# Kernel optimization log

Hardware: AMD Instinct MI355X
Metric: run time of the kernel (lower is better)

## Reference

```python
import jax, jax.numpy as jnp
import numpy as np

FRONT, END = 1, 2            # COMBINE_FRONT / COMBINE_END label values
BOS_ID, EOS_ID = 0, 1
BS, SLEN, D, H, L = 16, 256, 1024, 16, 2
N_POS = 512                  # N_MAX_POSITIONS


def setup_inputs():
    key = jax.random.key(0)
    ks = iter(jax.random.split(key, 80))
    nrm = lambda shape: jax.random.normal(next(ks), shape, dtype=jnp.float32) * 0.02
    inp = {}
    inp["encoded"] = jax.random.normal(next(ks), (BS, SLEN, D), dtype=jnp.float32)
    inp["lengths"] = jnp.full((BS,), SLEN, dtype=jnp.int32)  # assert slen == lengths.max()
    # deterministic valid word-span labels: [F,F,F,E,O,F,E,O] repeated -> words of 4 and 2 subwords
    pat = np.tile(np.array([1, 1, 1, 2, 0, 1, 2, 0], dtype=np.int32), SLEN // 8)
    inp["combine_labels"] = jnp.asarray(np.broadcast_to(pat, (BS, SLEN)).copy())
    inp["lang_id"] = 0
    inp["pos_emb"] = nrm((N_POS, D))
    inp["special_emb"] = nrm((3, D)).at[2].set(0.0)  # padding_idx=2 row zeroed
    for p in ("ctx", "wc"):
        for w in ("Wq", "Wk", "Wv", "Wo"):
            inp[p + "_" + w] = nrm((L, D, D))
        for b in ("bq", "bk", "bv", "bo", "b2", "be1", "be2"):
            inp[p + "_" + b] = jnp.zeros((L, D), dtype=jnp.float32)
        inp[p + "_W1"] = nrm((L, D, 4 * D))
        inp[p + "_b1"] = jnp.zeros((L, 4 * D), dtype=jnp.float32)
        inp[p + "_W2"] = nrm((L, 4 * D, D))
        inp[p + "_g1"] = jnp.ones((L, D), dtype=jnp.float32)
        inp[p + "_g2"] = jnp.ones((L, D), dtype=jnp.float32)
    return inp


def _ln(x, g, b):
    m = x.mean(-1, keepdims=True)
    v = ((x - m) ** 2).mean(-1, keepdims=True)
    return (x - m) / jnp.sqrt(v + 1e-5) * g + b


def _encoder(x, pad, P):
    # post-norm TransformerEncoder (torch default): attn -> add&LN -> relu-FFN -> add&LN
    Wq, Wk, Wv, Wo, bq, bk, bv, bo, W1, b1, W2, b2, g1, be1, g2, be2 = P
    B, S, Dm = x.shape
    hd = Dm // H
    scale = 1.0 / np.sqrt(hd)
    for i in range(Wq.shape[0]):
        q = (x @ Wq[i] + bq[i]).reshape(B, S, H, hd)
        k = (x @ Wk[i] + bk[i]).reshape(B, S, H, hd)
        v = (x @ Wv[i] + bv[i]).reshape(B, S, H, hd)
        s = jnp.einsum("bqhd,bkhd->bhqk", q, k) * scale
        s = jnp.where(pad[:, None, None, :], -1e9, s)  # src_key_padding_mask
        a = jax.nn.softmax(s, axis=-1)
        o = jnp.einsum("bhqk,bkhd->bqhd", a, v).reshape(B, S, Dm) @ Wo[i] + bo[i]
        x = _ln(x + o, g1[i], be1[i])
        h = jax.nn.relu(x @ W1[i] + b1[i]) @ W2[i] + b2[i]
        x = _ln(x + h, g2[i], be2[i])
    return x


def _word_inputs(encoded, combine_labels, special_emb):
    # vectorized replacement of the nested python-loop ragged span builder;
    # index math on the (concrete) labels in numpy, gathers/scatters in jnp.
    cl = np.asarray(combine_labels)
    f = cl == FRONT
    e = cl == END
    c = np.cumsum(f.astype(np.int64), axis=1)
    frontrun = c - np.maximum.accumulate(np.where(f, 0, c), axis=1)  # run of FRONTs ending here
    fr_prev = np.pad(frontrun[:, :-1], ((0, 0), (1, 0)))
    slot = np.where(f, frontrun, fr_prev + 1)  # 1-based slot inside word (slot 0 = BOS)
    e_flat = e.reshape(-1)
    wid = np.cumsum(e_flat) - e_flat  # word id = #ENDs strictly before, row-major order
    tok_idx = np.nonzero((f | e).reshape(-1))[0]
    w_tok = wid[tok_idx]
    s_tok = slot.reshape(-1)[tok_idx]
    wlen = fr_prev[e] + 3  # k subwords (fr_prev+1) + BOS + EOS
    n_word = wlen.shape[0]
    maxL = int(wlen.max())
    Dm = encoded.shape[-1]
    x = jnp.zeros((n_word, maxL, Dm), dtype=encoded.dtype)
    x = x.at[:, 0].set(special_emb[BOS_ID])
    x = x.at[np.arange(n_word), wlen - 1].set(special_emb[EOS_ID])  # eos at slot k+1
    x = x.at[w_tok, s_tok].set(encoded.reshape(-1, Dm)[tok_idx])
    return x, wlen


def _forward(encoded, lengths, combine_labels, pos_emb, special_emb, ctx, wc):
    S = encoded.shape[1]
    pad = jnp.asarray(np.arange(S)[None, :] >= np.asarray(lengths)[:, None])
    x = _encoder(encoded + pos_emb[:S][None], pad, ctx)          # another_encode
    winp, wlen = _word_inputs(x, combine_labels, special_emb)    # ragged gather, [n_word, maxL, D]
    maxL = winp.shape[1]
    wpad = jnp.asarray(np.arange(maxL)[None, :] >= wlen[:, None])
    y = _encoder(winp + pos_emb[:maxL][None], wpad, wc)          # word_encode
    return y[:, 0]  # position-0 (BOS) representation, [n_word, D]


def reference(encoded, lengths, combine_labels, lang_id, pos_emb, special_emb,
              ctx_Wq, ctx_Wk, ctx_Wv, ctx_Wo, ctx_bq, ctx_bk, ctx_bv, ctx_bo,
              ctx_W1, ctx_b1, ctx_W2, ctx_b2, ctx_g1, ctx_be1, ctx_g2, ctx_be2,
              wc_Wq, wc_Wk, wc_Wv, wc_Wo, wc_bq, wc_bk, wc_bv, wc_bo,
              wc_W1, wc_b1, wc_W2, wc_b2, wc_g1, wc_be1, wc_g2, wc_be2):
    ctx = (ctx_Wq, ctx_Wk, ctx_Wv, ctx_Wo, ctx_bq, ctx_bk, ctx_bv, ctx_bo,
           ctx_W1, ctx_b1, ctx_W2, ctx_b2, ctx_g1, ctx_be1, ctx_g2, ctx_be2)
    wc = (wc_Wq, wc_Wk, wc_Wv, wc_Wo, wc_bq, wc_bk, wc_bv, wc_bo,
          wc_W1, wc_b1, wc_W2, wc_b2, wc_g1, wc_be1, wc_g2, wc_be2)
    return _forward(encoded, lengths, combine_labels, pos_emb, special_emb, ctx, wc)
```

## Files before the change

kernel.cpp:

```cpp
#include <hip/hip_runtime.h>
#include <stdint.h>

typedef unsigned short u16;
typedef __attribute__((ext_vector_type(8))) short short8;
typedef __attribute__((ext_vector_type(4))) short short4v;
typedef __attribute__((ext_vector_type(4))) float f32x4;

#define DEV static __device__ __forceinline__

constexpr int B = 16, S = 256, D = 1024, H = 16, LYR = 2, FF = 4096;
constexpr int Mc = B * S;
constexpr int MAXL = 6;
constexpr int QKVS = 3 * D;

DEV u16 f2b(float f) {
  union { float f; uint32_t u; } a; a.f = f;
  uint32_t r = a.u + 0x7fffu + ((a.u >> 16) & 1u);
  return (u16)(r >> 16);
}
DEV float b2f(u16 b) {
  union { uint32_t u; float f; } a; a.u = ((uint32_t)b) << 16;
  return a.f;
}

DEV void glds16(const u16* g, u16* l) {
  __builtin_amdgcn_global_load_lds((const __attribute__((address_space(1))) void*)g,
                                   (__attribute__((address_space(3))) void*)l, 16, 0, 0);
}

struct TBatch {
  const float* src[6];
  u16* dst[6];
  int Kd[6];
  int Nd[6];
  int base[6];
};

__global__ __launch_bounds__(256) void transpose_batch(TBatch tb, int unused) {
  __shared__ float tile[64][65];
  const int bid = blockIdx.x;
  int wi = 0;
#pragma unroll
  for (int i = 1; i < 6; i++)
    if (bid >= tb.base[i]) wi = i;
  const float* __restrict__ W = tb.src[wi];
  u16* __restrict__ Wt = tb.dst[wi];
  const int K = tb.Kd[wi], N = tb.Nd[wi];
  const int local = bid - tb.base[wi];
  const int ntx = N >> 6;
  const int bn = (local % ntx) * 64, bk = (local / ntx) * 64;
  const int t = threadIdx.x;
  const int lr = t >> 2, lc = (t & 3) * 16;
#pragma unroll
  for (int q = 0; q < 4; q++) {
    float4 v = *(const float4*)&W[(size_t)(bk + lr) * N + bn + lc + q * 4];
    *(float4*)&tile[lr][lc + q * 4] = v;
  }
  __syncthreads();
  const int k0 = (t & 7) * 8;
#pragma unroll
  for (int p = 0; p < 2; p++) {
    const int n = (t >> 3) + p * 32;
    short8 o;
#pragma unroll
    for (int j = 0; j < 8; j++) o[j] = (short)f2b(tile[k0 + j][n]);
    *(short8*)&Wt[(size_t)(bn + n) * K + bk + k0] = o;
  }
}


template <int PASSES>
DEV void stage_rows(const u16* P, int lda, int k0, u16* Dst, int t) {
#pragma unroll
  for (int p = 0; p < PASSES; p++)
    glds16(P + (size_t)(p * 32) * lda + k0, Dst + p * 2048 + t * 8);
}

DEV void compute_tile(const u16* Asb, const u16* Bsb, f32x4 (&acc)[4][8],
                      int wm, int wn, int li, int hi) {
#pragma unroll
  for (int ks = 0; ks < 2; ks++) {
    const int ch = ((((ks << 2) | hi) ^ (li & 7)) * 8);
    short8 af[4], bfr[8];
#pragma unroll
    for (int i = 0; i < 4; i++)
      af[i] = *(const short8*)&Asb[(wm + i * 16 + li) * 64 + ch];
#pragma unroll
    for (int j = 0; j < 8; j++)
      bfr[j] = *(const short8*)&Bsb[(wn + j * 16 + li) * 64 + ch];
#pragma unroll
    for (int i = 0; i < 4; i++)
#pragma unroll
      for (int j = 0; j < 8; j++)
        acc[i][j] = __builtin_amdgcn_mfma_f32_16x16x32_bf16(af[i], bfr[j], acc[i][j], 0, 0, 0);
  }
}

template <int EPI, bool SPLITB, bool SPLITK>
__global__ __launch_bounds__(256, 2) void gemm_bt(const u16* __restrict__ A,
                                                  const u16* __restrict__ Bt,
                                                  const float* __restrict__ bias0,
                                                  const float* __restrict__ bias1,
                                                  const float* __restrict__ bias2,
                                                  u16* __restrict__ Cb,
                                                  int M, int N, int K, int lda, int NB) {
  __shared__ u16 As[128 * 64];
  __shared__ u16 Bs[256 * 64];
  const int t = threadIdx.x, lane = t & 63, w = t >> 6;
  const int wm = (w >> 1) * 64, wn = (w & 1) * 128;
  const int nwg = gridDim.x;
  const int cpx = nwg >> 3;
  const int swz = (blockIdx.x & 7) * cpx + (blockIdx.x >> 3);
  int sblk = 0, rem = swz;
  if (SPLITK) {
    const int tps = nwg >> 1;
    sblk = (swz >= tps) ? 1 : 0;
    rem = swz - sblk * tps;
  }
  const int n0 = (rem % NB) * 256, m0 = (rem / NB) * 128;
  const int pr = t >> 3;
  const int scb = (((t & 7) ^ (pr & 7)) * 8);
  f32x4 acc[4][8] = {};
  const u16* Ap = A + (size_t)sblk * K + (size_t)(m0 + pr) * lda + scb;
  const u16* Bp = Bt + (size_t)sblk * K + (size_t)(n0 + pr) * lda + scb;
  const int li = lane & 15, hi = lane >> 4;

  for (int k0 = 0; k0 < K; k0 += 64) {
    stage_rows<4>(Ap, lda, k0, &As[0], t);
    stage_rows<8>(Bp, lda, k0, &Bs[0], t);
    __syncthreads();
    compute_tile(&As[0], &Bs[0], acc, wm, wn, li, hi);
    __syncthreads();
  }

  u16* Cbs = Cb;
  if (SPLITK && EPI == 3) Cbs = Cb + (size_t)sblk * M * N;
  const int rg = hi * 4;
#pragma unroll
  for (int j = 0; j < 8; j++) {
    const int col = n0 + wn + j * 16 + li;
    float bv = 0.f;
    if (EPI != 3)
      bv = SPLITB ? (col < 1024 ? bias0 : col < 2048 ? bias1 : bias2)[col & 1023]
                  : bias0[col];
#pragma unroll
    for (int i = 0; i < 4; i++) {
      const int row0 = m0 + wm + i * 16 + rg;
#pragma unroll
      for (int r = 0; r < 4; r++) {
        float v = acc[i][j][r] + bv;
        if (EPI == 2) v = fmaxf(v, 0.f);
        Cbs[(size_t)(row0 + r) * N + col] = f2b(v);
      }
    }
  }
}

__global__ __launch_bounds__(256) void transpose_v(const u16* __restrict__ QKV,
                                                   u16* __restrict__ Vt) {
  const int kb = blockIdx.x, h = blockIdx.y, b = blockIdx.z;
  __shared__ u16 tile[64][72];
  const int t = threadIdx.x, lr = t >> 3, lc = (t & 7) * 8;
#pragma unroll
  for (int p = 0; p < 2; p++) {
    int r = lr + p * 32;
    *(short8*)&tile[r][lc] =
        *(const short8*)&QKV[(size_t)(b * 256 + kb * 64 + r) * QKVS + 2048 + h * 64 + lc];
  }
  __syncthreads();
#pragma unroll
  for (int p = 0; p < 2; p++) {
    int hd = lr + p * 32;
    short8 v8;
#pragma unroll
    for (int j = 0; j < 8; j++) v8[j] = (short)tile[lc + j][hd];
    *(short8*)&Vt[(size_t)((b * 16 + h) * 64 + hd) * 256 + kb * 64 + lc] = v8;
  }
}

__global__ __launch_bounds__(256) void attn_ctx(const u16* __restrict__ QKV,
                                                const u16* __restrict__ Vt,
                                                u16* __restrict__ AO,
                                                const int* __restrict__ lengths) {
  const int qt = blockIdx.x, h = blockIdx.y, b = blockIdx.z;
  __shared__ u16 Qs[64 * 64], Ks[64 * 64], Vs[64 * 64], Ps[64 * 64];
  const int t = threadIdx.x, lane = t & 63, w = t >> 6;
  const int len = lengths[b];
  const bool full = (len >= 256);
  const int lr = t >> 3, lc = (t & 7) * 8;
#pragma unroll
  for (int p = 0; p < 2; p++) {
    int r = lr + p * 32;
    *(short8*)&Qs[r * 64 + lc] =
        *(const short8*)&QKV[(size_t)(b * 256 + qt * 64 + r) * QKVS + h * 64 + lc];
  }
  const int li = lane & 15, kk = (lane >> 4) * 8, rg = (lane >> 4) * 4;
  float mrun[4], lrun[4];
  f32x4 oacc[4] = {};
#pragma unroll
  for (int r = 0; r < 4; r++) { mrun[r] = -1e30f; lrun[r] = 0.f; }

  for (int kt = 0; kt < 4; kt++) {
    __syncthreads();
#pragma unroll
    for (int p = 0; p < 2; p++) {
      int r = lr + p * 32;
      *(short8*)&Ks[r * 64 + lc] =
          *(const short8*)&QKV[(size_t)(b * 256 + kt * 64 + r) * QKVS + 1024 + h * 64 + lc];
      *(short8*)&Vs[r * 64 + lc] =
          *(const short8*)&Vt[(size_t)((b * 16 + h) * 64 + r) * 256 + kt * 64 + lc];
    }
    __syncthreads();
    f32x4 s[4] = {};
    short8 aq0 = *(const short8*)&Qs[(w * 16 + li) * 64 + kk];
    short8 aq1 = *(const short8*)&Qs[(w * 16 + li) * 64 + 32 + kk];
    __builtin_amdgcn_s_setprio(1);
#pragma unroll
    for (int fn = 0; fn < 4; fn++) {
      short8 b0 = *(const short8*)&Ks[(fn * 16 + li) * 64 + kk];
      short8 b1 = *(const short8*)&Ks[(fn * 16 + li) * 64 + 32 + kk];
      s[fn] = __builtin_amdgcn_mfma_f32_16x16x32_bf16(aq0, b0, s[fn], 0, 0, 0);
      s[fn] = __builtin_amdgcn_mfma_f32_16x16x32_bf16(aq1, b1, s[fn], 0, 0, 0);
    }
    __builtin_amdgcn_s_setprio(0);
    float pv[4][4];
    if (full) {
#pragma unroll
      for (int r = 0; r < 4; r++) {
        float mx = -1e30f;
#pragma unroll
        for (int fn = 0; fn < 4; fn++) {
          float v = s[fn][r] * 0.125f;
          pv[fn][r] = v;
          mx = fmaxf(mx, v);
        }
#pragma unroll
        for (int d = 1; d < 16; d <<= 1) mx = fmaxf(mx, __shfl_xor(mx, d));
        if (mx > mrun[r] + 8.f) {
          float sf = __expf(mrun[r] - mx);
          mrun[r] = mx;
          lrun[r] *= sf;
#pragma unroll
          for (int fn = 0; fn < 4; fn++) oacc[fn][r] *= sf;
        }
        float rs = 0.f;
#pragma unroll
        for (int fn = 0; fn < 4; fn++) {
          float p = __expf(pv[fn][r] - mrun[r]);
          pv[fn][r] = p;
          rs += p;
        }
#pragma unroll
        for (int d = 1; d < 16; d <<= 1) rs += __shfl_xor(rs, d);
        lrun[r] += rs;
      }
    } else {
#pragma unroll
      for (int r = 0; r < 4; r++) {
        float mx = -1e30f;
#pragma unroll
        for (int fn = 0; fn < 4; fn++) {
          int key = kt * 64 + fn * 16 + li;
          float v = (key < len) ? s[fn][r] * 0.125f : -1e30f;
          pv[fn][r] = v;
          mx = fmaxf(mx, v);
        }
#pragma unroll
        for (int d = 1; d < 16; d <<= 1) mx = fmaxf(mx, __shfl_xor(mx, d));
        float mnew = fmaxf(mrun[r], mx);
        float sf = __expf(mrun[r] - mnew);
        mrun[r] = mnew;
        float rs = 0.f;
#pragma unroll
        for (int fn = 0; fn < 4; fn++) {
          int key = kt * 64 + fn * 16 + li;
          float p = (key < len) ? __expf(pv[fn][r] - mnew) : 0.f;
          pv[fn][r] = p;
          rs += p;
        }
#pragma unroll
        for (int d = 1; d < 16; d <<= 1) rs += __shfl_xor(rs, d);
        lrun[r] = lrun[r] * sf + rs;
#pragma unroll
        for (int fn = 0; fn < 4; fn++) oacc[fn][r] *= sf;
      }
    }
#pragma unroll
    for (int fn = 0; fn < 4; fn++)
#pragma unroll
      for (int r = 0; r < 4; r++)
        Ps[(w * 16 + rg + r) * 64 + fn * 16 + li] = f2b(pv[fn][r]);
    __builtin_amdgcn_s_setprio(1);
#pragma unroll
    for (int ks = 0; ks < 2; ks++) {
      short8 ap = *(const short8*)&Ps[(w * 16 + li) * 64 + ks * 32 + kk];
#pragma unroll
      for (int fn = 0; fn < 4; fn++) {
        short8 bv = *(const short8*)&Vs[(fn * 16 + li) * 64 + ks * 32 + kk];
        oacc[fn] = __builtin_amdgcn_mfma_f32_16x16x32_bf16(ap, bv, oacc[fn], 0, 0, 0);
      }
    }
    __builtin_amdgcn_s_setprio(0);
  }
#pragma unroll
  for (int r = 0; r < 4; r++) {
    float inv = 1.f / fmaxf(lrun[r], 1e-30f);
    int row = b * 256 + qt * 64 + w * 16 + rg + r;
#pragma unroll
    for (int fn = 0; fn < 4; fn++) {
      int col = h * 64 + fn * 16 + li;
      AO[(size_t)row * 1024 + col] = f2b(oacc[fn][r] * inv);
    }
  }
}

__global__ __launch_bounds__(256) void attn_word(const u16* __restrict__ QKV,
                                                 const int* __restrict__ wlen,
                                                 u16* __restrict__ AO, int NW) {
  const int idx = blockIdx.x * 256 + threadIdx.x;
  if (idx >= NW * 16 * MAXL) return;
  const int i = idx % MAXL, h = (idx / MAXL) % 16, wd = idx / (MAXL * 16);
  const int len = wlen[wd];
  const size_t rowb = (size_t)(wd * MAXL + i) * QKVS;
  float q[64];
#pragma unroll
  for (int d = 0; d < 64; d += 8) {
    short8 q8 = *(const short8*)&QKV[rowb + h * 64 + d];
#pragma unroll
    for (int e = 0; e < 8; e++) q[d + e] = b2f((u16)q8[e]);
  }
  float sc[MAXL];
  float mx = -1e30f;
  for (int j = 0; j < MAXL; j++) {
    if (j >= len) { sc[j] = -1e30f; continue; }
    const size_t koff = (size_t)(wd * MAXL + j) * QKVS + 1024 + h * 64;
    float dot = 0.f;
#pragma unroll
    for (int d = 0; d < 64; d += 8) {
      short8 k8 = *(const short8*)&QKV[koff + d];
#pragma unroll
      for (int e = 0; e < 8; e++) dot += q[d + e] * b2f((u16)k8[e]);
    }
    sc[j] = dot * 0.125f;
    mx = fmaxf(mx, sc[j]);
  }
  float p[MAXL], l = 0.f;
  for (int j = 0; j < MAXL; j++) {
    p[j] = (j < len) ? __expf(sc[j] - mx) : 0.f;
    l += p[j];
  }
  const float rl = 1.f / fmaxf(l, 1e-30f);
  for (int j = 0; j < MAXL; j++) p[j] *= rl;
#pragma unroll
  for (int d = 0; d < 64; d += 8) {
    float acc[8] = {};
    for (int j = 0; j < MAXL; j++) {
      if (j >= len) break;
      short8 v8 = *(const short8*)&QKV[(size_t)(wd * MAXL + j) * QKVS + 2048 + h * 64 + d];
#pragma unroll
      for (int e = 0; e < 8; e++) acc[e] += p[j] * b2f((u16)v8[e]);
    }
    short8 o8;
#pragma unroll
    for (int e = 0; e < 8; e++) o8[e] = (short)f2b(acc[e]);
    *(short8*)&AO[(size_t)(wd * MAXL + i) * 1024 + h * 64 + d] = o8;
  }
}

template <bool WF32>
__global__ __launch_bounds__(256) void ln_resid2(const u16* __restrict__ Xin,
                                                 const u16* __restrict__ P0,
                                                 const u16* __restrict__ P1,
                                                 const float* __restrict__ bias,
                                                 const float* __restrict__ g,
                                                 const float* __restrict__ be,
                                                 u16* __restrict__ Xbo,
                                                 float* __restrict__ Xo) {
  const int row = blockIdx.x, t = threadIdx.x;
  const size_t base = (size_t)row * 1024 + t * 4;
  short4v x4 = *(const short4v*)&Xin[base];
  short4v p0 = *(const short4v*)&P0[base];
  short4v p1 = *(const short4v*)&P1[base];
  float4 bb = *(const float4*)&bias[t * 4];
  float v[4];
  v[0] = b2f((u16)x4[0]) + b2f((u16)p0[0]) + b2f((u16)p1[0]) + bb.x;
  v[1] = b2f((u16)x4[1]) + b2f((u16)p0[1]) + b2f((u16)p1[1]) + bb.y;
  v[2] = b2f((u16)x4[2]) + b2f((u16)p0[2]) + b2f((u16)p1[2]) + bb.z;
  v[3] = b2f((u16)x4[3]) + b2f((u16)p0[3]) + b2f((u16)p1[3]) + bb.w;
  float s = v[0] + v[1] + v[2] + v[3];
  float q = v[0] * v[0] + v[1] * v[1] + v[2] * v[2] + v[3] * v[3];
#pragma unroll
  for (int d = 1; d < 64; d <<= 1) { s += __shfl_xor(s, d); q += __shfl_xor(q, d); }
  __shared__ float ss[4], qq[4];
  if ((t & 63) == 0) { ss[t >> 6] = s; qq[t >> 6] = q; }
  __syncthreads();
  s = ss[0] + ss[1] + ss[2] + ss[3];
  q = qq[0] + qq[1] + qq[2] + qq[3];
  const float mean = s * (1.f / 1024.f);
  const float var = q * (1.f / 1024.f) - mean * mean;
  const float rstd = rsqrtf(var + 1e-5f);
  float4 gv = *(const float4*)&g[t * 4];
  float4 bv = *(const float4*)&be[t * 4];
  float y[4];
  y[0] = (v[0] - mean) * rstd * gv.x + bv.x;
  y[1] = (v[1] - mean) * rstd * gv.y + bv.y;
  y[2] = (v[2] - mean) * rstd * gv.z + bv.z;
  y[3] = (v[3] - mean) * rstd * gv.w + bv.w;
  if (WF32) *(float4*)&Xo[base] = make_float4(y[0], y[1], y[2], y[3]);
  short4v o = { (short)f2b(y[0]), (short)f2b(y[1]), (short)f2b(y[2]), (short)f2b(y[3]) };
  *(short4v*)&Xbo[base] = o;
}

__global__ __launch_bounds__(256) void posadd(const float* __restrict__ enc,
                                              const float* __restrict__ pos,
                                              u16* __restrict__ Xb) {
  const int row = blockIdx.x, t = threadIdx.x;
  const int sp = row & 255;
  const size_t base = (size_t)row * 1024 + t * 4;
  float4 e = *(const float4*)&enc[base];
  float4 p = *(const float4*)&pos[(size_t)sp * 1024 + t * 4];
  short4v o = { (short)f2b(e.x + p.x), (short)f2b(e.y + p.y),
                (short)f2b(e.z + p.z), (short)f2b(e.w + p.w) };
  *(short4v*)&Xb[base] = o;
}

__global__ void scan_words(const int* __restrict__ labels, int* __restrict__ t2w,
                           int* __restrict__ t2s, int* __restrict__ wlen) {
  __shared__ int rowEnds[16], rowBase[16];
  const int t = threadIdx.x;
  if (t < 16) {
    int c = 0;
    for (int s = 0; s < 256; s++) c += (labels[t * 256 + s] == 2);
    rowEnds[t] = c;
  }
  __syncthreads();
  if (t == 0) {
    int acc = 0;
    for (int b2 = 0; b2 < 16; b2++) { rowBase[b2] = acc; acc += rowEnds[b2]; }
  }
  __syncthreads();
  if (t < 16) {
    int wc = rowBase[t], fr = 0;
    for (int s = 0; s < 256; s++) {
      const int tok = t * 256 + s, lb = labels[tok];
      if (lb == 1) { fr++; t2w[tok] = wc; t2s[tok] = fr; }
      else if (lb == 2) { t2w[tok] = wc; t2s[tok] = fr + 1; wlen[wc] = fr + 3; wc++; fr = 0; }
      else { t2w[tok] = -1; t2s[tok] = 0; fr = 0; }
    }
  }
}

__global__ __launch_bounds__(256) void build_winp(const float* __restrict__ pos,
                                                  const float* __restrict__ spec,
                                                  const int* __restrict__ wlen,
                                                  u16* __restrict__ Xb) {
  const int row = blockIdx.x;
  const int wd = row / MAXL, sl = row % MAXL;
  const int len = wlen[wd];
  const int t = threadIdx.x;
  const size_t cb = t * 4;
  float4 p = *(const float4*)&pos[(size_t)sl * 1024 + cb];
  float4 e = make_float4(0.f, 0.f, 0.f, 0.f);
  if (sl == 0) e = *(const float4*)&spec[cb];
  else if (sl == len - 1) e = *(const float4*)&spec[1024 + cb];
  short4v o = { (short)f2b(p.x + e.x), (short)f2b(p.y + e.y),
                (short)f2b(p.z + e.z), (short)f2b(p.w + e.w) };
  *(short4v*)&Xb[(size_t)row * 1024 + cb] = o;
}

__global__ __launch_bounds__(256) void scatter_tokens(const u16* __restrict__ XcB,
                                                      const int* __restrict__ t2w,
                                                      const int* __restrict__ t2s,
                                                      u16* __restrict__ XW) {
  const int tok = blockIdx.x;
  const int wd = t2w[tok];
  if (wd < 0) return;
  const int row = wd * MAXL + t2s[tok];
  const size_t cb = threadIdx.x * 4;
  short4v a = *(const short4v*)&XcB[(size_t)tok * 1024 + cb];
  u16* dst = &XW[(size_t)row * 1024 + cb];
  short4v b2 = *(const short4v*)dst;
  short4v o;
#pragma unroll
  for (int e = 0; e < 4; e++) o[e] = (short)f2b(b2f((u16)a[e]) + b2f((u16)b2[e]));
  *(short4v*)dst = o;
}

__global__ __launch_bounds__(256) void gather_out(const float* __restrict__ XW,
                                                  float* __restrict__ out) {
  const int wd = blockIdx.x;
  const size_t cb = threadIdx.x * 4;
  *(float4*)&out[(size_t)wd * 1024 + cb] =
      *(const float4*)&XW[(size_t)(wd * MAXL) * 1024 + cb];
}

extern "C" void kernel_launch(void* const* d_in, const int* in_sizes, int n_in,
                              void* d_out, int out_size, void* d_ws, size_t ws_size,
                              hipStream_t stream) {
  const float* encoded = (const float*)d_in[0];
  const int* lengths = (const int*)d_in[1];
  const int* labels = (const int*)d_in[2];
  const float* pos = (const float*)d_in[4];
  const float* spec = (const float*)d_in[5];
  const float* W[2][16];
  for (int p = 0; p < 2; p++)
    for (int i = 0; i < 16; i++) W[p][i] = (const float*)d_in[6 + p * 16 + i];

  const int NW = out_size / D;
  const int Mw = NW * MAXL;

  char* wp = (char*)d_ws;
  size_t off = 0;
  auto alloc = [&](size_t bytes) {
    void* r = wp + off;
    off += (bytes + 255) & ~(size_t)255;
    return r;
  };
  float* x_word = (float*)alloc((size_t)Mw * D * 4);
  u16* xb_ctx = (u16*)alloc((size_t)Mc * D * 2);
  u16* xb_word = (u16*)alloc((size_t)Mw * D * 2);
  u16* wtQKV = (u16*)alloc((size_t)3 * D * D * 2);
  u16* wtO = (u16*)alloc((size_t)D * D * 2);
  u16* wtW1 = (u16*)alloc((size_t)D * FF * 2);
  u16* wtW2 = (u16*)alloc((size_t)D * FF * 2);
  char* uni = (char*)alloc((size_t)Mw * FF * 2);
  u16* QKV = (u16*)uni;
  u16* Vt = (u16*)(uni + ((size_t)40 << 20));
  u16* hb = (u16*)uni;
  u16* AOb = (u16*)alloc((size_t)Mw * D * 2);
  u16* tmpb = (u16*)alloc((size_t)2 * Mw * D * 2);
  int* t2w = (int*)alloc((size_t)Mc * 4);
  int* t2s = (int*)alloc((size_t)Mc * 4);
  int* wlen = (int*)alloc((size_t)NW * 4);
  (void)ws_size; (void)in_sizes; (void)n_in;

  posadd<<<Mc, 256, 0, stream>>>(encoded, pos, xb_ctx);

  auto run_encoder = [&](int p, u16* xb, int M, bool is_ctx) {
    for (int l = 0; l < LYR; l++) {
      const size_t oDD = (size_t)l * D * D, oDF = (size_t)l * D * FF;
      const bool final_ln = (!is_ctx) && (l == LYR - 1);
      TBatch tb;
      tb.src[0] = W[p][0] + oDD; tb.dst[0] = wtQKV;               tb.Kd[0] = D;  tb.Nd[0] = D;
      tb.src[1] = W[p][1] + oDD; tb.dst[1] = wtQKV + (size_t)D * D;   tb.Kd[1] = D;  tb.Nd[1] = D;
      tb.src[2] = W[p][2] + oDD; tb.dst[2] = wtQKV + (size_t)2 * D * D; tb.Kd[2] = D; tb.Nd[2] = D;
      tb.src[3] = W[p][3] + oDD; tb.dst[3] = wtO;                 tb.Kd[3] = D;  tb.Nd[3] = D;
      tb.src[4] = W[p][11] + oDF; tb.dst[4] = wtW1;               tb.Kd[4] = D;  tb.Nd[4] = FF;
      tb.src[5] = W[p][13] + oDF; tb.dst[5] = wtW2;               tb.Kd[5] = FF; tb.Nd[5] = D;
      int base = 0;
      for (int i = 0; i < 6; i++) {
        tb.base[i] = base;
        base += (tb.Kd[i] / 64) * (tb.Nd[i] / 64);
      }
      transpose_batch<<<base, 256, 0, stream>>>(tb, 0);

      gemm_bt<1, true, false><<<(3 * D / 256) * (M / 128), 256, 0, stream>>>(
          xb, wtQKV, W[p][4] + (size_t)l * D, W[p][5] + (size_t)l * D,
          W[p][6] + (size_t)l * D, QKV, M, 3 * D, D, D, 3 * D / 256);
      if (is_ctx) {
        transpose_v<<<dim3(4, H, B), 256, 0, stream>>>(QKV, Vt);
        attn_ctx<<<dim3(4, H, B), 256, 0, stream>>>(QKV, Vt, AOb, lengths);
      } else {
        attn_word<<<(NW * H * MAXL + 255) / 256, 256, 0, stream>>>(QKV, wlen, AOb, NW);
      }
      gemm_bt<3, false, true><<<2 * (D / 256) * (M / 128), 256, 0, stream>>>(
          AOb, wtO, nullptr, nullptr, nullptr, tmpb, M, D, 512, D, D / 256);
      ln_resid2<false><<<M, 256, 0, stream>>>(xb, tmpb, tmpb + (size_t)M * D,
                                              W[p][7] + (size_t)l * D, W[p][14] + (size_t)l * D,
                                              W[p][9] + (size_t)l * D, xb, nullptr);
      gemm_bt<2, false, false><<<(FF / 256) * (M / 128), 256, 0, stream>>>(
          xb, wtW1, W[p][12] + (size_t)l * FF, nullptr, nullptr, hb, M, FF, D, D, FF / 256);
      gemm_bt<3, false, true><<<2 * (D / 256) * (M / 128), 256, 0, stream>>>(
          hb, wtW2, nullptr, nullptr, nullptr, tmpb, M, D, 2048, FF, D / 256);
      if (final_ln)
        ln_resid2<true><<<M, 256, 0, stream>>>(xb, tmpb, tmpb + (size_t)M * D,
                                               W[p][8] + (size_t)l * D, W[p][15] + (size_t)l * D,
                                               W[p][10] + (size_t)l * D, xb, x_word);
      else
        ln_resid2<false><<<M, 256, 0, stream>>>(xb, tmpb, tmpb + (size_t)M * D,
                                                W[p][8] + (size_t)l * D, W[p][15] + (size_t)l * D,
                                                W[p][10] + (size_t)l * D, xb, nullptr);
    }
  };

  run_encoder(0, xb_ctx, Mc, true);

  scan_words<<<1, 64, 0, stream>>>(labels, t2w, t2s, wlen);
  build_winp<<<Mw, 256, 0, stream>>>(pos, spec, wlen, xb_word);
  scatter_tokens<<<Mc, 256, 0, stream>>>(xb_ctx, t2w, t2s, xb_word);

  run_encoder(1, xb_word, Mw, false);

  gather_out<<<NW, 256, 0, stream>>>(x_word, (float*)d_out);
}
```

Before: 976.9 us.

## Compute only BOS rows after QKV in final word-encoder layer

The last word-encoder layer only needs each word's position-0 output. After the full QKV projection, attention, the O projection, both layer norms and the FFN now run only on the NW BOS rows instead of NW*MAXL rows, and the final LN writes straight to the output. This drops the separate gather kernel and most of the last layer's FFN/O-proj work. It adds separate A/B leading-dimension arguments to the GEMM and a row stride to the LN kernel. NW must be a multiple of 128 for the GEMM tiling.

```diff
diff --git a/kernel.cpp b/kernel.cpp
--- a/kernel.cpp
+++ b/kernel.cpp
@@ -103,7 +103,8 @@
                                                   const float* __restrict__ bias1,
                                                   const float* __restrict__ bias2,
                                                   u16* __restrict__ Cb,
-                                                  int M, int N, int K, int lda, int NB) {
+                                                  int M, int N, int K, int ldaA, int ldaB,
+                                                  int NB) {
   __shared__ u16 As[128 * 64];
   __shared__ u16 Bs[256 * 64];
   const int t = threadIdx.x, lane = t & 63, w = t >> 6;
@@ -121,13 +122,13 @@
   const int pr = t >> 3;
   const int scb = (((t & 7) ^ (pr & 7)) * 8);
   f32x4 acc[4][8] = {};
-  const u16* Ap = A + (size_t)sblk * K + (size_t)(m0 + pr) * lda + scb;
-  const u16* Bp = Bt + (size_t)sblk * K + (size_t)(n0 + pr) * lda + scb;
+  const u16* Ap = A + (size_t)sblk * K + (size_t)(m0 + pr) * ldaA + scb;
+  const u16* Bp = Bt + (size_t)sblk * K + (size_t)(n0 + pr) * ldaB + scb;
   const int li = lane & 15, hi = lane >> 4;
 
   for (int k0 = 0; k0 < K; k0 += 64) {
-    stage_rows<4>(Ap, lda, k0, &As[0], t);
-    stage_rows<8>(Bp, lda, k0, &Bs[0], t);
+    stage_rows<4>(Ap, ldaA, k0, &As[0], t);
+    stage_rows<8>(Bp, ldaB, k0, &Bs[0], t);
     __syncthreads();
     compute_tile(&As[0], &Bs[0], acc, wm, wn, li, hi);
     __syncthreads();
@@ -367,7 +368,60 @@
   }
 }
 
-template <bool WF32>
+__global__ __launch_bounds__(256) void attn_word_bos(const u16* __restrict__ QKV,
+                                                     const int* __restrict__ wlen,
+                                                     u16* __restrict__ AOc, int NW) {
+  const int idx = blockIdx.x * 256 + threadIdx.x;
+  if (idx >= NW * 16) return;
+  const int h = idx % 16, wd = idx / 16;
+  const int len = wlen[wd];
+  const size_t rowb = (size_t)(wd * MAXL) * QKVS;
+  float q[64];
+#pragma unroll
+  for (int d = 0; d < 64; d += 8) {
+    short8 q8 = *(const short8*)&QKV[rowb + h * 64 + d];
+#pragma unroll
+    for (int e = 0; e < 8; e++) q[d + e] = b2f((u16)q8[e]);
+  }
+  float sc[MAXL];
+  float mx = -1e30f;
+  for (int j = 0; j < MAXL; j++) {
+    if (j >= len) { sc[j] = -1e30f; continue; }
+    const size_t koff = (size_t)(wd * MAXL + j) * QKVS + 1024 + h * 64;
+    float dot = 0.f;
+#pragma unroll
+    for (int d = 0; d < 64; d += 8) {
+      short8 k8 = *(const short8*)&QKV[koff + d];
+#pragma unroll
+      for (int e = 0; e < 8; e++) dot += q[d + e] * b2f((u16)k8[e]);
+    }
+    sc[j] = dot * 0.125f;
+    mx = fmaxf(mx, sc[j]);
+  }
+  float p[MAXL], l = 0.f;
+  for (int j = 0; j < MAXL; j++) {
+    p[j] = (j < len) ? __expf(sc[j] - mx) : 0.f;
+    l += p[j];
+  }
+  const float rl = 1.f / fmaxf(l, 1e-30f);
+  for (int j = 0; j < MAXL; j++) p[j] *= rl;
+#pragma unroll
+  for (int d = 0; d < 64; d += 8) {
+    float acc[8] = {};
+    for (int j = 0; j < MAXL; j++) {
+      if (j >= len) break;
+      short8 v8 = *(const short8*)&QKV[(size_t)(wd * MAXL + j) * QKVS + 2048 + h * 64 + d];
+#pragma unroll
+      for (int e = 0; e < 8; e++) acc[e] += p[j] * b2f((u16)v8[e]);
+    }
+    short8 o8;
+#pragma unroll
+    for (int e = 0; e < 8; e++) o8[e] = (short)f2b(acc[e]);
+    *(short8*)&AOc[(size_t)wd * 1024 + h * 64 + d] = o8;
+  }
+}
+
+template <int RS, bool WF32>
 __global__ __launch_bounds__(256) void ln_resid2(const u16* __restrict__ Xin,
                                                  const u16* __restrict__ P0,
                                                  const u16* __restrict__ P1,
@@ -378,7 +432,8 @@
                                                  float* __restrict__ Xo) {
   const int row = blockIdx.x, t = threadIdx.x;
   const size_t base = (size_t)row * 1024 + t * 4;
-  short4v x4 = *(const short4v*)&Xin[base];
+  const size_t basein = (size_t)row * RS * 1024 + t * 4;
+  short4v x4 = *(const short4v*)&Xin[basein];
   short4v p0 = *(const short4v*)&P0[base];
   short4v p1 = *(const short4v*)&P1[base];
   float4 bb = *(const float4*)&bias[t * 4];
@@ -486,14 +541,6 @@
   *(short4v*)dst = o;
 }
 
-__global__ __launch_bounds__(256) void gather_out(const float* __restrict__ XW,
-                                                  float* __restrict__ out) {
-  const int wd = blockIdx.x;
-  const size_t cb = threadIdx.x * 4;
-  *(float4*)&out[(size_t)wd * 1024 + cb] =
-      *(const float4*)&XW[(size_t)(wd * MAXL) * 1024 + cb];
-}
-
 extern "C" void kernel_launch(void* const* d_in, const int* in_sizes, int n_in,
                               void* d_out, int out_size, void* d_ws, size_t ws_size,
                               hipStream_t stream) {
@@ -516,9 +563,9 @@
     off += (bytes + 255) & ~(size_t)255;
     return r;
   };
-  float* x_word = (float*)alloc((size_t)Mw * D * 4);
   u16* xb_ctx = (u16*)alloc((size_t)Mc * D * 2);
   u16* xb_word = (u16*)alloc((size_t)Mw * D * 2);
+  u16* xc = (u16*)alloc((size_t)NW * D * 2);
   u16* wtQKV = (u16*)alloc((size_t)3 * D * D * 2);
   u16* wtO = (u16*)alloc((size_t)D * D * 2);
   u16* wtW1 = (u16*)alloc((size_t)D * FF * 2);
@@ -536,60 +583,75 @@
 
   posadd<<<Mc, 256, 0, stream>>>(encoded, pos, xb_ctx);
 
-  auto run_encoder = [&](int p, u16* xb, int M, bool is_ctx) {
-    for (int l = 0; l < LYR; l++) {
-      const size_t oDD = (size_t)l * D * D, oDF = (size_t)l * D * FF;
-      const bool final_ln = (!is_ctx) && (l == LYR - 1);
-      TBatch tb;
-      tb.src[0] = W[p][0] + oDD; tb.dst[0] = wtQKV;               tb.Kd[0] = D;  tb.Nd[0] = D;
-      tb.src[1] = W[p][1] + oDD; tb.dst[1] = wtQKV + (size_t)D * D;   tb.Kd[1] = D;  tb.Nd[1] = D;
-      tb.src[2] = W[p][2] + oDD; tb.dst[2] = wtQKV + (size_t)2 * D * D; tb.Kd[2] = D; tb.Nd[2] = D;
-      tb.src[3] = W[p][3] + oDD; tb.dst[3] = wtO;                 tb.Kd[3] = D;  tb.Nd[3] = D;
-      tb.src[4] = W[p][11] + oDF; tb.dst[4] = wtW1;               tb.Kd[4] = D;  tb.Nd[4] = FF;
-      tb.src[5] = W[p][13] + oDF; tb.dst[5] = wtW2;               tb.Kd[5] = FF; tb.Nd[5] = D;
-      int base = 0;
-      for (int i = 0; i < 6; i++) {
-        tb.base[i] = base;
-        base += (tb.Kd[i] / 64) * (tb.Nd[i] / 64);
-      }
-      transpose_batch<<<base, 256, 0, stream>>>(tb, 0);
-
-      gemm_bt<1, true, false><<<(3 * D / 256) * (M / 128), 256, 0, stream>>>(
-          xb, wtQKV, W[p][4] + (size_t)l * D, W[p][5] + (size_t)l * D,
-          W[p][6] + (size_t)l * D, QKV, M, 3 * D, D, D, 3 * D / 256);
-      if (is_ctx) {
-        transpose_v<<<dim3(4, H, B), 256, 0, stream>>>(QKV, Vt);
-        attn_ctx<<<dim3(4, H, B), 256, 0, stream>>>(QKV, Vt, AOb, lengths);
-      } else {
-        attn_word<<<(NW * H * MAXL + 255) / 256, 256, 0, stream>>>(QKV, wlen, AOb, NW);
-      }
-      gemm_bt<3, false, true><<<2 * (D / 256) * (M / 128), 256, 0, stream>>>(
-          AOb, wtO, nullptr, nullptr, nullptr, tmpb, M, D, 512, D, D / 256);
-      ln_resid2<false><<<M, 256, 0, stream>>>(xb, tmpb, tmpb + (size_t)M * D,
-                                              W[p][7] + (size_t)l * D, W[p][14] + (size_t)l * D,
-                                              W[p][9] + (size_t)l * D, xb, nullptr);
-      gemm_bt<2, false, false><<<(FF / 256) * (M / 128), 256, 0, stream>>>(
-          xb, wtW1, W[p][12] + (size_t)l * FF, nullptr, nullptr, hb, M, FF, D, D, FF / 256);
-      gemm_bt<3, false, true><<<2 * (D / 256) * (M / 128), 256, 0, stream>>>(
-          hb, wtW2, nullptr, nullptr, nullptr, tmpb, M, D, 2048, FF, D / 256);
-      if (final_ln)
-        ln_resid2<true><<<M, 256, 0, stream>>>(xb, tmpb, tmpb + (size_t)M * D,
+  auto transpose_layer = [&](int p, int l) {
+    const size_t oDD = (size_t)l * D * D, oDF = (size_t)l * D * FF;
+    TBatch tb;
+    tb.src[0] = W[p][0] + oDD; tb.dst[0] = wtQKV;                 tb.Kd[0] = D;  tb.Nd[0] = D;
+    tb.src[1] = W[p][1] + oDD; tb.dst[1] = wtQKV + (size_t)D * D; tb.Kd[1] = D;  tb.Nd[1] = D;
+    tb.src[2] = W[p][2] + oDD; tb.dst[2] = wtQKV + (size_t)2 * D * D; tb.Kd[2] = D; tb.Nd[2] = D;
+    tb.src[3] = W[p][3] + oDD; tb.dst[3] = wtO;                   tb.Kd[3] = D;  tb.Nd[3] = D;
+    tb.src[4] = W[p][11] + oDF; tb.dst[4] = wtW1;                 tb.Kd[4] = D;  tb.Nd[4] = FF;
+    tb.src[5] = W[p][13] + oDF; tb.dst[5] = wtW2;                 tb.Kd[5] = FF; tb.Nd[5] = D;
+    int base = 0;
+    for (int i = 0; i < 6; i++) {
+      tb.base[i] = base;
+      base += (tb.Kd[i] / 64) * (tb.Nd[i] / 64);
+    }
+    transpose_batch<<<base, 256, 0, stream>>>(tb, 0);
+  };
+
+  auto full_layer = [&](int p, int l, u16* xb, int M, bool is_ctx) {
+    transpose_layer(p, l);
+    gemm_bt<1, true, false><<<(3 * D / 256) * (M / 128), 256, 0, stream>>>(
+        xb, wtQKV, W[p][4] + (size_t)l * D, W[p][5] + (size_t)l * D,
+        W[p][6] + (size_t)l * D, QKV, M, 3 * D, D, D, D, 3 * D / 256);
+    if (is_ctx) {
+      transpose_v<<<dim3(4, H, B), 256, 0, stream>>>(QKV, Vt);
+      attn_ctx<<<dim3(4, H, B), 256, 0, stream>>>(QKV, Vt, AOb, lengths);
+    } else {
+      attn_word<<<(NW * H * MAXL + 255) / 256, 256, 0, stream>>>(QKV, wlen, AOb, NW);
+    }
+    gemm_bt<3, false, true><<<2 * (D / 256) * (M / 128), 256, 0, stream>>>(
+        AOb, wtO, nullptr, nullptr, nullptr, tmpb, M, D, 512, D, D, D / 256);
+    ln_resid2<1, false><<<M, 256, 0, stream>>>(xb, tmpb, tmpb + (size_t)M * D,
+                                               W[p][7] + (size_t)l * D, W[p][14] + (size_t)l * D,
+                                               W[p][9] + (size_t)l * D, xb, nullptr);
+    gemm_bt<2, false, false><<<(FF / 256) * (M / 128), 256, 0, stream>>>(
+        xb, wtW1, W[p][12] + (size_t)l * FF, nullptr, nullptr, hb, M, FF, D, D, D, FF / 256);
+    gemm_bt<3, false, true><<<2 * (D / 256) * (M / 128), 256, 0, stream>>>(
+        hb, wtW2, nullptr, nullptr, nullptr, tmpb, M, D, 2048, FF, FF, D / 256);
+    ln_resid2<1, false><<<M, 256, 0, stream>>>(xb, tmpb, tmpb + (size_t)M * D,
                                                W[p][8] + (size_t)l * D, W[p][15] + (size_t)l * D,
-                                               W[p][10] + (size_t)l * D, xb, x_word);
-      else
-        ln_resid2<false><<<M, 256, 0, stream>>>(xb, tmpb, tmpb + (size_t)M * D,
-                                                W[p][8] + (size_t)l * D, W[p][15] + (size_t)l * D,
-                                                W[p][10] + (size_t)l * D, xb, nullptr);
-    }
+                                               W[p][10] + (size_t)l * D, xb, nullptr);
   };
 
-  run_encoder(0, xb_ctx, Mc, true);
+  full_layer(0, 0, xb_ctx, Mc, true);
+  full_layer(0, 1, xb_ctx, Mc, true);
 
   scan_words<<<1, 64, 0, stream>>>(labels, t2w, t2s, wlen);
   build_winp<<<Mw, 256, 0, stream>>>(pos, spec, wlen, xb_word);
   scatter_tokens<<<Mc, 256, 0, stream>>>(xb_ctx, t2w, t2s, xb_word);
 
-  run_encoder(1, xb_word, Mw, false);
-
-  gather_out<<<NW, 256, 0, stream>>>(x_word, (float*)d_out);
-}
+  full_layer(1, 0, xb_word, Mw, false);
+
+  {
+    const int p = 1, l = 1;
+    transpose_layer(p, l);
+    gemm_bt<1, true, false><<<(3 * D / 256) * (Mw / 128), 256, 0, stream>>>(
+        xb_word, wtQKV, W[p][4] + (size_t)l * D, W[p][5] + (size_t)l * D,
+        W[p][6] + (size_t)l * D, QKV, Mw, 3 * D, D, D, D, 3 * D / 256);
+    attn_word_bos<<<(NW * H + 255) / 256, 256, 0, stream>>>(QKV, wlen, AOb, NW);
+    gemm_bt<3, false, true><<<2 * (D / 256) * (NW / 128), 256, 0, stream>>>(
+        AOb, wtO, nullptr, nullptr, nullptr, tmpb, NW, D, 512, D, D, D / 256);
+    ln_resid2<MAXL, false><<<NW, 256, 0, stream>>>(
+        xb_word, tmpb, tmpb + (size_t)NW * D, W[p][7] + (size_t)l * D,
+        W[p][14] + (size_t)l * D, W[p][9] + (size_t)l * D, xc, nullptr);
+    gemm_bt<2, false, false><<<(FF / 256) * (NW / 128), 256, 0, stream>>>(
+        xc, wtW1, W[p][12] + (size_t)l * FF, nullptr, nullptr, hb, NW, FF, D, D, D, FF / 256);
+    gemm_bt<3, false, true><<<2 * (D / 256) * (NW / 128), 256, 0, stream>>>(
+        hb, wtW2, nullptr, nullptr, nullptr, tmpb, NW, D, 2048, FF, FF, D / 256);
+    ln_resid2<1, true><<<NW, 256, 0, stream>>>(
+        xc, tmpb, tmpb + (size_t)NW * D, W[p][8] + (size_t)l * D,
+        W[p][15] + (size_t)l * D, W[p][10] + (size_t)l * D, xc, (float*)d_out);
+  }
+}
```

After: 913.2 us. 1.07x faster.
